# Optimization experiments

Measured on AMD Instinct MI355X. Metric: run time of the kernel, lower is better.

## Reference

```python
import jax, jax.numpy as jnp
import numpy as np

NUM_LEAVES = 256
EPS = 1e-6
SHARPNESS = 1.0   # init_sharpness, non-trainable buffer
BIAS_SHIFT = -2.0


def _generalized_gcd(w1, w2, lambd):
    # lambd: per-node bias -> andness via sigmoid; broadcast over batch
    lam = jax.nn.sigmoid(lambd)
    a = jnp.abs(w1) + EPS
    b = jnp.abs(w2) + EPS
    return lam * jnp.minimum(a, b) + (1.0 - lam) * jnp.maximum(a, b)


def setup_inputs() -> dict:
    key = jax.random.key(0)
    ks = jax.random.split(key, 6)
    B, L = 65536, NUM_LEAVES
    x = jax.random.normal(ks[0], (B, L), jnp.float32)
    # xavier-like scale for the leaf projection
    W_leaf = jax.random.normal(ks[1], (L, L), jnp.float32) * (1.0 / np.sqrt(L))
    weights = jax.random.uniform(ks[2], (L - 1, 2), jnp.float32, 0.5, 1.5)
    biases = jax.random.uniform(ks[3], (L - 1,), jnp.float32) * 0.1
    w_out = jax.random.normal(ks[4], (1, 1), jnp.float32)
    b_out = jnp.full((1,), 0.5, jnp.float32)
    return {"x": x, "W_leaf": W_leaf, "weights": weights,
            "biases": biases, "w_out": w_out, "b_out": b_out}


def reference(x, W_leaf, weights, biases, w_out, b_out):
    # InputToLeafFC: sigmoid(sharpness * (x @ W^T + bias_shift))
    leaf = jax.nn.sigmoid(SHARPNESS * (x @ W_leaf.T + BIAS_SHIFT))  # (B, L)

    # The original pops two nodes from the front of the queue and appends the
    # result; for a power-of-two leaf count this is exactly a level-by-level
    # pairwise tree reduction, with node weights consumed in order.
    cur = leaf
    off = 0
    n = cur.shape[1]
    while n > 1:  # log2(L) levels, each fully vectorized over (batch, pairs)
        m = n // 2
        w = weights[off:off + m]   # (m, 2)
        b = biases[off:off + m]    # (m,)
        left = cur[:, 0::2] * w[:, 0]
        right = cur[:, 1::2] * w[:, 1]
        cur = _generalized_gcd(left, right, b)  # (B, m)
        off += m
        n = m
    # fc_out: Linear(1,1) then sigmoid -> (B, 1)
    return jax.nn.sigmoid(cur * w_out[0, 0] + b_out[0])
```

## Files before the change

kernel.cpp:

```cpp
#include <hip/hip_runtime.h>
#include <stdint.h>


#define EPS 1e-6f
#define LOG2E 1.44269504088896340736f
#define PARAM_OFF 131072

typedef __attribute__((ext_vector_type(8))) short short8;
typedef __attribute__((ext_vector_type(4))) short short4_t;
typedef __attribute__((ext_vector_type(4))) float float4_t;

__device__ __forceinline__ float fast_sigmoid(float z) {
    float e = __builtin_amdgcn_exp2f(-z * LOG2E);
    return __builtin_amdgcn_rcpf(1.0f + e);
}

__device__ __forceinline__ short f2bf(float f) {
    uint32_t u = __builtin_bit_cast(uint32_t, f);
    u += 0x7FFFu + ((u >> 16) & 1u);
    return (short)(u >> 16);
}

__device__ __forceinline__ short8 pack8(float4 a, float4 b) {
    short8 s;
    s[0] = f2bf(a.x); s[1] = f2bf(a.y); s[2] = f2bf(a.z); s[3] = f2bf(a.w);
    s[4] = f2bf(b.x); s[5] = f2bf(b.y); s[6] = f2bf(b.z); s[7] = f2bf(b.w);
    return s;
}

__device__ __forceinline__ float ggcd(float l, float r, float lam) {
    float a = fabsf(l) + EPS;
    float b = fabsf(r) + EPS;
    float mn = fminf(a, b);
    float mx = fmaxf(a, b);
    return fmaf(lam, mn - mx, mx);
}

__device__ __forceinline__ void lds16(const void* g, void* l) {
    __builtin_amdgcn_global_load_lds(
        (const __attribute__((address_space(1))) unsigned int*)g,
        (__attribute__((address_space(3))) unsigned int*)l, 16, 0, 0);
}

__device__ __forceinline__ void tree_reduce(float4_t acc[16], int c0,
                                            const float4* pv, float res[4]) {
    #pragma unroll
    for (int t = 0; t < 16; ++t) {
        #pragma unroll
        for (int r = 0; r < 4; ++r) acc[t][r] = fast_sigmoid(acc[t][r] - 2.0f);
    }
    #pragma unroll
    for (int tp = 0; tp < 8; ++tp) {
        float4 p = pv[c0 * 8 + tp];
        #pragma unroll
        for (int r = 0; r < 4; ++r)
            acc[tp][r] = ggcd(acc[2*tp][r] * p.x, acc[2*tp+1][r] * p.y, p.z);
    }
    #pragma unroll
    for (int tp = 0; tp < 4; ++tp) {
        float4 p = pv[128 + c0 * 4 + tp];
        #pragma unroll
        for (int r = 0; r < 4; ++r)
            acc[tp][r] = ggcd(acc[2*tp][r] * p.x, acc[2*tp+1][r] * p.y, p.z);
    }
    #pragma unroll
    for (int tp = 0; tp < 2; ++tp) {
        float4 p = pv[192 + c0 * 2 + tp];
        #pragma unroll
        for (int r = 0; r < 4; ++r)
            acc[tp][r] = ggcd(acc[2*tp][r] * p.x, acc[2*tp+1][r] * p.y, p.z);
    }
    {
        float4 p = pv[224 + c0];
        #pragma unroll
        for (int r = 0; r < 4; ++r)
            res[r] = ggcd(acc[0][r] * p.x, acc[1][r] * p.y, p.z);
    }
}

__global__ __launch_bounds__(256)
void convert_w(const float* __restrict__ Wl, const float* __restrict__ wts,
               const float* __restrict__ bia, char* __restrict__ img) {
    int i = blockIdx.x * 256 + threadIdx.x;
    int a = i * 8;
    int kt   = a >> 15;
    int s    = a & 32767;
    int j    = s >> 7;
    int b    = s & 127;
    int cpos = b >> 4;
    int h    = (b >> 3) & 1;
    int c    = cpos ^ (j & 7);
    int k    = kt * 64 + c * 8 + h * 4;
    int src  = ((j & 15) << 4) | (j >> 4);
    float4 w4 = *(const float4*)&Wl[src * 256 + k];
    short4_t s4;
    s4.x = f2bf(w4.x); s4.y = f2bf(w4.y); s4.z = f2bf(w4.z); s4.w = f2bf(w4.w);
    *(short4_t*)&img[a] = s4;

    if (i < 255) {
        float4* pv = (float4*)(img + PARAM_OFF);
        pv[i] = make_float4(wts[2 * i], wts[2 * i + 1], fast_sigmoid(bia[i]), 0.f);
    } else if (i == 255) {
        ((float4*)(img + PARAM_OFF))[255] = make_float4(0.f, 0.f, 0.f, 0.f);
    }
}

__global__ __launch_bounds__(512, 4)
void btln_main(const float* __restrict__ x, const char* __restrict__ img,
               const float* __restrict__ wout, const float* __restrict__ bout,
               float* __restrict__ out) {
    __shared__ short Wt[2][16384];
    __shared__ float4 pv[256];

    const int tid  = threadIdx.x;
    const int lane = tid & 63;
    const int wv   = tid >> 6;
    const int c0   = lane & 15;
    const int q    = lane >> 4;

    if (tid < 256) pv[tid] = ((const float4*)(img + PARAM_OFF))[tid];

    {
        const char* g = img + wv * 4096 + lane * 16;
        char* l = (char*)&Wt[0][wv * 2048];
        #pragma unroll
        for (int it = 0; it < 4; ++it)
            lds16(g + it * 1024, l + it * 1024);
    }

    const int rowbase = blockIdx.x * 128 + wv * 16;
    const float* xr = x + (size_t)(rowbase + c0) * 256;

    float4_t acc[16];
    #pragma unroll
    for (int t = 0; t < 16; ++t) acc[t] = (float4_t){0.f, 0.f, 0.f, 0.f};

    float4 a0 = *(const float4*)(xr + q * 8);
    float4 a1 = *(const float4*)(xr + q * 8 + 4);
    float4 a2 = *(const float4*)(xr + 32 + q * 8);
    float4 a3 = *(const float4*)(xr + 32 + q * 8 + 4);

    __syncthreads();

    const int vx = c0 & 7;
    #pragma unroll 1
    for (int kt = 0; kt < 4; ++kt) {
        const short* cur = Wt[kt & 1];
        if (kt < 3) {
            const char* g = img + (kt + 1) * 32768 + wv * 4096 + lane * 16;
            char* l = (char*)&Wt[(kt + 1) & 1][wv * 2048];
            #pragma unroll
            for (int it = 0; it < 4; ++it)
                lds16(g + it * 1024, l + it * 1024);
        }
        const int kn = (kt < 3 ? kt + 1 : 3) * 64;
        float4 b0 = *(const float4*)(xr + kn + q * 8);
        float4 b1 = *(const float4*)(xr + kn + q * 8 + 4);
        float4 b2 = *(const float4*)(xr + kn + 32 + q * 8);
        float4 b3 = *(const float4*)(xr + kn + 32 + q * 8 + 4);

        short8 af0 = pack8(a0, a1);
        short8 af1 = pack8(a2, a3);
        #pragma unroll
        for (int t = 0; t < 16; ++t) {
            const short* base = &cur[(t * 16 + c0) * 64];
            short8 bf0 = *(const short8*)&base[(q ^ vx) * 8];
            short8 bf1 = *(const short8*)&base[((q + 4) ^ vx) * 8];
            acc[t] = __builtin_amdgcn_mfma_f32_16x16x32_bf16(af0, bf0, acc[t], 0, 0, 0);
            acc[t] = __builtin_amdgcn_mfma_f32_16x16x32_bf16(af1, bf1, acc[t], 0, 0, 0);
        }
        __syncthreads();
        a0 = b0; a1 = b1; a2 = b2; a3 = b3;
    }

    float res[4];
    tree_reduce(acc, c0, pv, res);

    const int offs[4] = {240, 248, 252, 254};
    #pragma unroll
    for (int k = 0; k < 4; ++k) {
        float4 p = pv[offs[k] + (c0 >> (k + 1))];
        bool isLeft = ((c0 >> k) & 1) == 0;
        #pragma unroll
        for (int r = 0; r < 4; ++r) {
            float other = __shfl_xor(res[r], 1 << k, 64);
            float lf = isLeft ? res[r] : other;
            float rt = isLeft ? other  : res[r];
            res[r] = ggcd(lf * p.x, rt * p.y, p.z);
        }
    }

    if (c0 == 0) {
        const float wo = wout[0];
        const float bo = bout[0];
        #pragma unroll
        for (int r = 0; r < 4; ++r)
            out[rowbase + q * 4 + r] = fast_sigmoid(fmaf(res[r], wo, bo));
    }
}

extern "C" void kernel_launch(void* const* d_in, const int* in_sizes, int n_in,
                              void* d_out, int out_size, void* d_ws, size_t ws_size,
                              hipStream_t stream) {
    const float* x   = (const float*)d_in[0];
    const float* Wl  = (const float*)d_in[1];
    const float* wts = (const float*)d_in[2];
    const float* bia = (const float*)d_in[3];
    const float* wo  = (const float*)d_in[4];
    const float* bo  = (const float*)d_in[5];
    float* out = (float*)d_out;
    char* img = (char*)d_ws;

    convert_w<<<dim3(64), dim3(256), 0, stream>>>(Wl, wts, bia, img);

    const int rows = out_size;
    dim3 grid(rows / 128), block(512);
    btln_main<<<grid, block, 0, stream>>>(x, img, wo, bo, out);
}
```

Before: 113.7 us.

## Pre-convert x to bf16 in a prep kernel before the GEMM-tree kernel

```diff
diff --git a/kernel.cpp b/kernel.cpp
--- a/kernel.cpp
+++ b/kernel.cpp
@@ -4,6 +4,8 @@
 
 #define EPS 1e-6f
 #define LOG2E 1.44269504088896340736f
+#define XIMG_BYTES (65536ull * 256ull * 2ull)
+#define WOFF XIMG_BYTES
 #define PARAM_OFF 131072
 
 typedef __attribute__((ext_vector_type(8))) short short8;
@@ -19,13 +21,6 @@
     uint32_t u = __builtin_bit_cast(uint32_t, f);
     u += 0x7FFFu + ((u >> 16) & 1u);
     return (short)(u >> 16);
-}
-
-__device__ __forceinline__ short8 pack8(float4 a, float4 b) {
-    short8 s;
-    s[0] = f2bf(a.x); s[1] = f2bf(a.y); s[2] = f2bf(a.z); s[3] = f2bf(a.w);
-    s[4] = f2bf(b.x); s[5] = f2bf(b.y); s[6] = f2bf(b.z); s[7] = f2bf(b.w);
-    return s;
 }
 
 __device__ __forceinline__ float ggcd(float l, float r, float lam) {
@@ -79,38 +74,58 @@
 }
 
 __global__ __launch_bounds__(256)
-void convert_w(const float* __restrict__ Wl, const float* __restrict__ wts,
-               const float* __restrict__ bia, char* __restrict__ img) {
-    int i = blockIdx.x * 256 + threadIdx.x;
-    int a = i * 8;
-    int kt   = a >> 15;
-    int s    = a & 32767;
-    int j    = s >> 7;
-    int b    = s & 127;
-    int cpos = b >> 4;
-    int h    = (b >> 3) & 1;
-    int c    = cpos ^ (j & 7);
-    int k    = kt * 64 + c * 8 + h * 4;
-    int src  = ((j & 15) << 4) | (j >> 4);
-    float4 w4 = *(const float4*)&Wl[src * 256 + k];
-    short4_t s4;
-    s4.x = f2bf(w4.x); s4.y = f2bf(w4.y); s4.z = f2bf(w4.z); s4.w = f2bf(w4.w);
-    *(short4_t*)&img[a] = s4;
-
-    if (i < 255) {
-        float4* pv = (float4*)(img + PARAM_OFF);
-        pv[i] = make_float4(wts[2 * i], wts[2 * i + 1], fast_sigmoid(bia[i]), 0.f);
-    } else if (i == 255) {
-        ((float4*)(img + PARAM_OFF))[255] = make_float4(0.f, 0.f, 0.f, 0.f);
+void prep(const float* __restrict__ x, const float* __restrict__ Wl,
+          const float* __restrict__ wts, const float* __restrict__ bia,
+          char* __restrict__ ws) {
+    const int bid = blockIdx.x;
+    if (bid < 4096) {
+        const float4* xin = (const float4*)x;
+        short4_t* xout = (short4_t*)ws;
+        const int base = bid * 1024 + threadIdx.x;
+        #pragma unroll
+        for (int j = 0; j < 4; ++j) {
+            int i = base + j * 256;
+            float4 v = xin[i];
+            short4_t s4;
+            s4.x = f2bf(v.x); s4.y = f2bf(v.y); s4.z = f2bf(v.z); s4.w = f2bf(v.w);
+            xout[i] = s4;
+        }
+    } else {
+        char* img = ws + WOFF;
+        int i = (bid - 4096) * 256 + threadIdx.x;
+        int a = i * 8;
+        int kt   = a >> 15;
+        int s    = a & 32767;
+        int j    = s >> 7;
+        int b    = s & 127;
+        int cpos = b >> 4;
+        int h    = (b >> 3) & 1;
+        int c    = cpos ^ (j & 7);
+        int k    = kt * 64 + c * 8 + h * 4;
+        int src  = ((j & 15) << 4) | (j >> 4);
+        float4 w4 = *(const float4*)&Wl[src * 256 + k];
+        short4_t s4;
+        s4.x = f2bf(w4.x); s4.y = f2bf(w4.y); s4.z = f2bf(w4.z); s4.w = f2bf(w4.w);
+        *(short4_t*)&img[a] = s4;
+
+        if (i < 255) {
+            float4* pv = (float4*)(img + PARAM_OFF);
+            pv[i] = make_float4(wts[2 * i], wts[2 * i + 1], fast_sigmoid(bia[i]), 0.f);
+        } else if (i == 255) {
+            ((float4*)(img + PARAM_OFF))[255] = make_float4(0.f, 0.f, 0.f, 0.f);
+        }
     }
 }
 
 __global__ __launch_bounds__(512, 4)
-void btln_main(const float* __restrict__ x, const char* __restrict__ img,
+void btln_main(const char* __restrict__ ws,
                const float* __restrict__ wout, const float* __restrict__ bout,
                float* __restrict__ out) {
     __shared__ short Wt[2][16384];
     __shared__ float4 pv[256];
+
+    const short* x_bf = (const short*)ws;
+    const char*  img  = ws + WOFF;
 
     const int tid  = threadIdx.x;
     const int lane = tid & 63;
@@ -129,16 +144,14 @@
     }
 
     const int rowbase = blockIdx.x * 128 + wv * 16;
-    const float* xr = x + (size_t)(rowbase + c0) * 256;
+    const short8* xr8 = (const short8*)(x_bf + (size_t)(rowbase + c0) * 256);
 
     float4_t acc[16];
     #pragma unroll
     for (int t = 0; t < 16; ++t) acc[t] = (float4_t){0.f, 0.f, 0.f, 0.f};
 
-    float4 a0 = *(const float4*)(xr + q * 8);
-    float4 a1 = *(const float4*)(xr + q * 8 + 4);
-    float4 a2 = *(const float4*)(xr + 32 + q * 8);
-    float4 a3 = *(const float4*)(xr + 32 + q * 8 + 4);
+    short8 a0 = xr8[q];
+    short8 a1 = xr8[q + 4];
 
     __syncthreads();
 
@@ -153,24 +166,20 @@
             for (int it = 0; it < 4; ++it)
                 lds16(g + it * 1024, l + it * 1024);
         }
-        const int kn = (kt < 3 ? kt + 1 : 3) * 64;
-        float4 b0 = *(const float4*)(xr + kn + q * 8);
-        float4 b1 = *(const float4*)(xr + kn + q * 8 + 4);
-        float4 b2 = *(const float4*)(xr + kn + 32 + q * 8);
-        float4 b3 = *(const float4*)(xr + kn + 32 + q * 8 + 4);
-
-        short8 af0 = pack8(a0, a1);
-        short8 af1 = pack8(a2, a3);
+        const int kb = (kt < 3 ? kt + 1 : 3) * 8;
+        short8 n0 = xr8[kb + q];
+        short8 n1 = xr8[kb + 4 + q];
+
         #pragma unroll
         for (int t = 0; t < 16; ++t) {
             const short* base = &cur[(t * 16 + c0) * 64];
             short8 bf0 = *(const short8*)&base[(q ^ vx) * 8];
             short8 bf1 = *(const short8*)&base[((q + 4) ^ vx) * 8];
-            acc[t] = __builtin_amdgcn_mfma_f32_16x16x32_bf16(af0, bf0, acc[t], 0, 0, 0);
-            acc[t] = __builtin_amdgcn_mfma_f32_16x16x32_bf16(af1, bf1, acc[t], 0, 0, 0);
+            acc[t] = __builtin_amdgcn_mfma_f32_16x16x32_bf16(a0, bf0, acc[t], 0, 0, 0);
+            acc[t] = __builtin_amdgcn_mfma_f32_16x16x32_bf16(a1, bf1, acc[t], 0, 0, 0);
         }
         __syncthreads();
-        a0 = b0; a1 = b1; a2 = b2; a3 = b3;
+        a0 = n0; a1 = n1;
     }
 
     float res[4];
@@ -209,11 +218,11 @@
     const float* wo  = (const float*)d_in[4];
     const float* bo  = (const float*)d_in[5];
     float* out = (float*)d_out;
-    char* img = (char*)d_ws;
-
-    convert_w<<<dim3(64), dim3(256), 0, stream>>>(Wl, wts, bia, img);
+    char* ws = (char*)d_ws;
+
+    prep<<<dim3(4096 + 64), dim3(256), 0, stream>>>(x, Wl, wts, bia, ws);
 
     const int rows = out_size;
     dim3 grid(rows / 128), block(512);
-    btln_main<<<grid, block, 0, stream>>>(x, img, wo, bo, out);
-}
+    btln_main<<<grid, block, 0, stream>>>(ws, wo, bo, out);
+}
```

Result: slower. 126.3 us (+11.0%).

## Halve block size and K-tile depth to shrink LDS footprint per block

Applied to the files above, without the earlier changes.

```diff
diff --git a/kernel.cpp b/kernel.cpp
--- a/kernel.cpp
+++ b/kernel.cpp
@@ -83,14 +83,14 @@
                const float* __restrict__ bia, char* __restrict__ img) {
     int i = blockIdx.x * 256 + threadIdx.x;
     int a = i * 8;
-    int kt   = a >> 15;
-    int s    = a & 32767;
-    int j    = s >> 7;
-    int b    = s & 127;
+    int t    = a >> 14;
+    int s    = a & 16383;
+    int j    = s >> 6;
+    int b    = s & 63;
     int cpos = b >> 4;
     int h    = (b >> 3) & 1;
-    int c    = cpos ^ (j & 7);
-    int k    = kt * 64 + c * 8 + h * 4;
+    int c    = cpos ^ (j & 3);
+    int k    = t * 32 + c * 8 + h * 4;
     int src  = ((j & 15) << 4) | (j >> 4);
     float4 w4 = *(const float4*)&Wl[src * 256 + k];
     short4_t s4;
@@ -105,11 +105,11 @@
     }
 }
 
-__global__ __launch_bounds__(512, 4)
+__global__ __launch_bounds__(256, 4)
 void btln_main(const float* __restrict__ x, const char* __restrict__ img,
                const float* __restrict__ wout, const float* __restrict__ bout,
                float* __restrict__ out) {
-    __shared__ short Wt[2][16384];
+    __shared__ short Wt[2][8192];
     __shared__ float4 pv[256];
 
     const int tid  = threadIdx.x;
@@ -118,17 +118,13 @@
     const int c0   = lane & 15;
     const int q    = lane >> 4;
 
-    if (tid < 256) pv[tid] = ((const float4*)(img + PARAM_OFF))[tid];
-
-    {
-        const char* g = img + wv * 4096 + lane * 16;
-        char* l = (char*)&Wt[0][wv * 2048];
-        #pragma unroll
-        for (int it = 0; it < 4; ++it)
-            lds16(g + it * 1024, l + it * 1024);
-    }
-
-    const int rowbase = blockIdx.x * 128 + wv * 16;
+    pv[tid] = ((const float4*)(img + PARAM_OFF))[tid];
+
+    #pragma unroll
+    for (int p = 0; p < 4; ++p)
+        lds16(img + p * 4096 + tid * 16, (char*)Wt[0] + p * 4096 + tid * 16);
+
+    const int rowbase = blockIdx.x * 64 + wv * 16;
     const float* xr = x + (size_t)(rowbase + c0) * 256;
 
     float4_t acc[16];
@@ -137,40 +133,33 @@
 
     float4 a0 = *(const float4*)(xr + q * 8);
     float4 a1 = *(const float4*)(xr + q * 8 + 4);
-    float4 a2 = *(const float4*)(xr + 32 + q * 8);
-    float4 a3 = *(const float4*)(xr + 32 + q * 8 + 4);
 
     __syncthreads();
 
-    const int vx = c0 & 7;
+    const int vx = c0 & 3;
     #pragma unroll 1
-    for (int kt = 0; kt < 4; ++kt) {
+    for (int kt = 0; kt < 8; ++kt) {
         const short* cur = Wt[kt & 1];
-        if (kt < 3) {
-            const char* g = img + (kt + 1) * 32768 + wv * 4096 + lane * 16;
-            char* l = (char*)&Wt[(kt + 1) & 1][wv * 2048];
+        if (kt < 7) {
+            const char* g = img + (kt + 1) * 16384 + tid * 16;
+            char* l = (char*)Wt[(kt + 1) & 1] + tid * 16;
             #pragma unroll
-            for (int it = 0; it < 4; ++it)
-                lds16(g + it * 1024, l + it * 1024);
+            for (int p = 0; p < 4; ++p)
+                lds16(g + p * 4096, l + p * 4096);
         }
-        const int kn = (kt < 3 ? kt + 1 : 3) * 64;
-        float4 b0 = *(const float4*)(xr + kn + q * 8);
-        float4 b1 = *(const float4*)(xr + kn + q * 8 + 4);
-        float4 b2 = *(const float4*)(xr + kn + 32 + q * 8);
-        float4 b3 = *(const float4*)(xr + kn + 32 + q * 8 + 4);
-
-        short8 af0 = pack8(a0, a1);
-        short8 af1 = pack8(a2, a3);
+        const int kn = (kt < 7 ? kt + 1 : 7) * 32;
+        float4 n0 = *(const float4*)(xr + kn + q * 8);
+        float4 n1 = *(const float4*)(xr + kn + q * 8 + 4);
+
+        short8 af = pack8(a0, a1);
         #pragma unroll
         for (int t = 0; t < 16; ++t) {
-            const short* base = &cur[(t * 16 + c0) * 64];
-            short8 bf0 = *(const short8*)&base[(q ^ vx) * 8];
-            short8 bf1 = *(const short8*)&base[((q + 4) ^ vx) * 8];
-            acc[t] = __builtin_amdgcn_mfma_f32_16x16x32_bf16(af0, bf0, acc[t], 0, 0, 0);
-            acc[t] = __builtin_amdgcn_mfma_f32_16x16x32_bf16(af1, bf1, acc[t], 0, 0, 0);
+            const short* base = &cur[(t * 16 + c0) * 32];
+            short8 bf = *(const short8*)&base[(q ^ vx) * 8];
+            acc[t] = __builtin_amdgcn_mfma_f32_16x16x32_bf16(af, bf, acc[t], 0, 0, 0);
         }
         __syncthreads();
-        a0 = b0; a1 = b1; a2 = b2; a3 = b3;
+        a0 = n0; a1 = n1;
     }
 
     float res[4];
@@ -214,6 +203,6 @@
     convert_w<<<dim3(64), dim3(256), 0, stream>>>(Wl, wts, bia, img);
 
     const int rows = out_size;
-    dim3 grid(rows / 128), block(512);
+    dim3 grid(rows / 64), block(256);
     btln_main<<<grid, block, 0, stream>>>(x, img, wo, bo, out);
 }
```

New measurement: 118.0 us. +3.7%, slower.
